# Kernel tuning notes

Hardware: AMD Instinct MI355X
Metric: run time of the kernel (lower is better)

The kernel has to match this reference:

```python
import jax, jax.numpy as jnp
import numpy as np

KERNEL_SIZE = 257

def conv1d_same_padding(x, weights):
    # x: [B,1,L], weights: [K]  (cross-correlation, matching torch F.conv1d)
    K = weights.shape[0]
    pad_total = K - 1
    if pad_total % 2 != 0:
        x = jnp.pad(x, ((0, 0), (0, 0), (0, 1)))
    p = pad_total // 2
    w = weights.reshape(1, 1, K)  # [out_ch, in_ch, K]
    return jax.lax.conv_general_dilated(
        x, w, window_strides=(1,), padding=[(p, p)],
        dimension_numbers=('NCW', 'OIW', 'NCW'))

def topk_absolutes_1d(x, k):
    # keep top-k |values| per sample, zero the rest (scatter semantics of repo)
    B = x.shape[0]
    xf = x.reshape(B, -1)
    _, idx = jax.lax.top_k(jnp.abs(xf), k)            # [B, k]
    vals = jnp.take_along_axis(xf, idx, axis=-1)      # [B, k]
    out = jnp.zeros_like(xf).at[jnp.arange(B)[:, None], idx].set(vals)
    return out.reshape(x.shape)

def setup_inputs() -> dict:
    key = jax.random.key(0)
    k1, k2 = jax.random.split(key)
    x = jax.random.normal(k1, (64, 1, 262144), dtype=jnp.float32)
    weights = jax.random.normal(k2, (KERNEL_SIZE,), dtype=jnp.float32) * 0.1
    return {"x": x, "weights": weights, "k": 2048}

def reference(x, weights, k):
    similarity = conv1d_same_padding(x, weights)
    extrema = topk_absolutes_1d(similarity, k)
    reconstruction = conv1d_same_padding(extrema, weights)
    return (reconstruction, similarity, extrema)
```

## Files before the change

kernel.cpp:

```cpp
#include <hip/hip_runtime.h>

#define L_LEN 262144
#define KSZ 257
#define BLK 256
#define R 16
#define TILE (BLK * R)
#define HALO (KSZ - 1)
#define LDSA (TILE + HALO)
#define NBIN 4096
#define SEGCAP 256
#define NCHUNK 32
#define CANDMAX 4096
#define TIECAP 1024

#define LDSW 4368
#define NJ 9

typedef __attribute__((ext_vector_type(8))) short bf16x8;
typedef __attribute__((ext_vector_type(4))) float f32x4;

__device__ __forceinline__ ushort bf16_rne(float f) {
    const unsigned u = __float_as_uint(f);
    return (ushort)((u + 0x7FFFu + ((u >> 16) & 1u)) >> 16);
}

__global__ __launch_bounds__(BLK) void zero_ghist_kernel(uint4* __restrict__ p) {
    p[(size_t)blockIdx.x * BLK + threadIdx.x] = make_uint4(0u, 0u, 0u, 0u);
}

__global__ __launch_bounds__(BLK) void conv_hist_kernel(const float* __restrict__ in,
                                                        const float* __restrict__ w,
                                                        float* __restrict__ out,
                                                        unsigned* __restrict__ ghist) {
    __shared__ float lx[LDSA + LDSA / 16];
    __shared__ unsigned shist[NBIN];
    const int t = threadIdx.x;
    const int sample = blockIdx.x >> 6;
    const int tile   = blockIdx.x & 63;
    const float* xrow = in  + (size_t)sample * L_LEN;
    float*       orow = out + (size_t)sample * L_LEN;
    const int tstart = tile * TILE;
    const int gbase  = tstart - (KSZ / 2);

    for (int h = t; h < NBIN; h += BLK) shist[h] = 0u;

    for (int i4 = t; i4 < LDSA / 4; i4 += BLK) {
        const int g = gbase + i4 * 4;
        float4 v;
        if ((unsigned)g <= (unsigned)(L_LEN - 4)) v = *(const float4*)(xrow + g);
        else v = make_float4(0.f, 0.f, 0.f, 0.f);
        const int ib = i4 * 4;
        const int p = ib + (ib >> 4);
        lx[p]     = v.x; lx[p + 1] = v.y; lx[p + 2] = v.z; lx[p + 3] = v.w;
    }
    __syncthreads();

    const int pb = t * 17;
    float acc[R], win[R];
#pragma unroll
    for (int r = 0; r < R; ++r) acc[r] = 0.f;
#pragma unroll
    for (int p = 0; p < R; ++p) win[p] = lx[pb + p];

#pragma unroll 1
    for (int j0 = 0; j0 < KSZ - 1; j0 += R) {
        const int pj = pb + j0 + (j0 >> 4) + 17;
#pragma unroll
        for (int jj = 0; jj < R; ++jj) {
            const float wj = w[j0 + jj];
#pragma unroll
            for (int r = 0; r < R; ++r)
                acc[r] += win[(jj + r) & (R - 1)] * wj;
            win[jj] = lx[pj + jj];
        }
    }
    const float wl = w[KSZ - 1];
#pragma unroll
    for (int r = 0; r < R; ++r) acc[r] += win[r] * wl;

#pragma unroll
    for (int r4 = 0; r4 < R; r4 += 4)
        *(float4*)(orow + tstart + t * R + r4) =
            make_float4(acc[r4], acc[r4 + 1], acc[r4 + 2], acc[r4 + 3]);

#pragma unroll
    for (int r = 0; r < R; ++r) {
        const unsigned u = (__float_as_uint(acc[r]) & 0x7fffffffu) >> 19;
        atomicAdd(&shist[u], 1u);
    }
    __syncthreads();
    for (int h = t; h < NBIN; h += BLK) {
        const unsigned c = shist[h];
        if (c) atomicAdd(&ghist[(size_t)sample * NBIN + h], c);
    }
}

__global__ __launch_bounds__(BLK) void mfma_recon_kernel(const float* __restrict__ in,
                                                         const float* __restrict__ w,
                                                         float* __restrict__ out) {
    __shared__ ushort xh[LDSW];
    __shared__ ushort xl[LDSW];

    const int t = threadIdx.x;
    const int sample = blockIdx.x >> 6;
    const int tile   = blockIdx.x & 63;
    const float* xrow = in  + (size_t)sample * L_LEN;
    float*       orow = out + (size_t)sample * L_LEN;
    const int tstart = tile * TILE;
    const int gbase  = tstart - (KSZ / 2);

    for (int i4 = t; i4 < LDSW / 4; i4 += BLK) {
        const int g = gbase + i4 * 4;
        float4 v;
        if ((unsigned)g <= (unsigned)(L_LEN - 4)) v = *(const float4*)(xrow + g);
        else v = make_float4(0.f, 0.f, 0.f, 0.f);
        const float vv[4] = {v.x, v.y, v.z, v.w};
        ushort h4[4], l4[4];
#pragma unroll
        for (int e = 0; e < 4; ++e) {
            const ushort h = bf16_rne(vv[e]);
            h4[e] = h;
            l4[e] = bf16_rne(vv[e] - __uint_as_float((unsigned)h << 16));
        }
        *(ushort4*)(&xh[i4 * 4]) = make_ushort4(h4[0], h4[1], h4[2], h4[3]);
        *(ushort4*)(&xl[i4 * 4]) = make_ushort4(l4[0], l4[1], l4[2], l4[3]);
    }

    const int lane = t & 63;
    const int cc = lane & 15;
    const int bb = lane >> 4;
    bf16x8 Bh[NJ], Bl[NJ];
#pragma unroll
    for (int f = 0; f < NJ; ++f) {
#pragma unroll
        for (int e = 0; e < 8; ++e) {
            const int j = f * 32 + 8 * bb + e - cc;
            const float v = ((unsigned)j <= 256u) ? w[j] : 0.f;
            const ushort h = bf16_rne(v);
            Bh[f][e] = (short)h;
            Bl[f][e] = (short)bf16_rne(v - __uint_as_float((unsigned)h << 16));
        }
    }
    __syncthreads();

    const int wv = t >> 6;
    const int wvbase = wv * 1024;
    const int arow = 16 * cc + 8 * bb;

    f32x4 acc[4] = {};
#pragma unroll
    for (int f = 0; f < NJ; ++f) {
#pragma unroll
        for (int st = 0; st < 4; ++st) {
            const int ao = wvbase + st * 256 + f * 32 + arow;
            const bf16x8 Ah = *(const bf16x8*)(&xh[ao]);
            const bf16x8 Al = *(const bf16x8*)(&xl[ao]);
            acc[st] = __builtin_amdgcn_mfma_f32_16x16x32_bf16(Ah, Bh[f], acc[st], 0, 0, 0);
            acc[st] = __builtin_amdgcn_mfma_f32_16x16x32_bf16(Ah, Bl[f], acc[st], 0, 0, 0);
            acc[st] = __builtin_amdgcn_mfma_f32_16x16x32_bf16(Al, Bh[f], acc[st], 0, 0, 0);
        }
    }

#pragma unroll
    for (int st = 0; st < 4; ++st) {
        const int mbase = tstart + wvbase + st * 256 + 64 * bb + cc;
#pragma unroll
        for (int r = 0; r < 4; ++r)
            orow[mbase + 16 * r] = acc[st][r];
    }
}

__global__ __launch_bounds__(1024) void bin_select_kernel(const unsigned* __restrict__ ghist,
                                                          int2* __restrict__ sel,
                                                          const int* __restrict__ kptr) {
    __shared__ int ss[1024];
    const int t = threadIdx.x;
    const int b = blockIdx.x;
    const unsigned* hist = ghist + (size_t)b * NBIN;
    const int k = kptr[0];

    const int g4 = t * 4;
    const int h0 = (int)hist[g4], h1 = (int)hist[g4 + 1],
              h2 = (int)hist[g4 + 2], h3 = (int)hist[g4 + 3];
    ss[t] = h0 + h1 + h2 + h3;
    __syncthreads();
    for (int off = 1; off < 1024; off <<= 1) {
        const int add = (t + off < 1024) ? ss[t + off] : 0;
        __syncthreads();
        ss[t] += add;
        __syncthreads();
    }
    const int S0 = ss[t];
    const int S4 = (t < 1023) ? ss[t + 1] : 0;
    const int S1 = S0 - h0, S2 = S1 - h1, S3 = S2 - h2;
    if (S0 >= k && S1 < k) sel[b] = make_int2(g4,     k - S1);
    if (S1 >= k && S2 < k) sel[b] = make_int2(g4 + 1, k - S2);
    if (S2 >= k && S3 < k) sel[b] = make_int2(g4 + 2, k - S3);
    if (S3 >= k && S4 < k) sel[b] = make_int2(g4 + 3, k - S4);
}

__global__ __launch_bounds__(BLK) void write_gather_kernel(const float* __restrict__ sim,
                                                           float* __restrict__ ext,
                                                           uint2* __restrict__ cand,
                                                           int* __restrict__ segCnt,
                                                           const int2* __restrict__ sel) {
    __shared__ int s_cnt;
    const int t = threadIdx.x;
    const int b = blockIdx.x >> 5;
    const int chunk = blockIdx.x & (NCHUNK - 1);
    const unsigned selBin = (unsigned)sel[b].x;
    const float* row  = sim + (size_t)b * L_LEN;
    float*       erow = ext + (size_t)b * L_LEN;
    uint2* seg = cand + ((size_t)b * NCHUNK + chunk) * SEGCAP;
    const int base = chunk * (L_LEN / NCHUNK);

    if (t == 0) s_cnt = 0;
    __syncthreads();

    for (int i = t; i < (L_LEN / NCHUNK) / 4; i += BLK) {
        const int g = base + i * 4;
        const float4 v = *(const float4*)(row + g);
        const float vv[4] = {v.x, v.y, v.z, v.w};
        float o[4];
#pragma unroll
        for (int e = 0; e < 4; ++e) {
            const unsigned u = __float_as_uint(vv[e]) & 0x7fffffffu;
            const unsigned u12 = u >> 19;
            o[e] = (u12 > selBin) ? vv[e] : 0.f;
            if (u12 == selBin) {
                const int p = atomicAdd(&s_cnt, 1);
                if (p < SEGCAP) seg[p] = make_uint2(u, (unsigned)(g + e));
            }
        }
        *(float4*)(erow + g) = make_float4(o[0], o[1], o[2], o[3]);
    }
    __syncthreads();
    if (t == 0) segCnt[b * NCHUNK + chunk] = (s_cnt < SEGCAP) ? s_cnt : SEGCAP;
}

__global__ __launch_bounds__(1024) void finalize_kernel(const float* __restrict__ sim,
                                                        float* __restrict__ ext,
                                                        const uint2* __restrict__ cand,
                                                        const int* __restrict__ segCnt,
                                                        const int2* __restrict__ sel) {
    __shared__ int hist[1024];
    __shared__ int ss[1024];
    __shared__ uint2 list[CANDMAX];
    __shared__ int tie[TIECAP];
    __shared__ int scnt[NCHUNK];
    __shared__ int segoff[NCHUNK + 1];
    __shared__ int s_b1, s_kk2, s_Tlow, s_m, s_tieCnt;
    const int t = threadIdx.x;
    const int b = blockIdx.x;
    const float* srow = sim + (size_t)b * L_LEN;
    float*       erow = ext + (size_t)b * L_LEN;
    const int kk = sel[b].y;

    if (t < NCHUNK) scnt[t] = segCnt[b * NCHUNK + t];
    __syncthreads();
    if (t == 0) {
        int acc0 = 0;
        for (int s = 0; s < NCHUNK; ++s) { segoff[s] = acc0; acc0 += scnt[s]; }
        segoff[NCHUNK] = acc0;
    }
    if (t == 1) s_tieCnt = 0;
    __syncthreads();
    int cnt = segoff[NCHUNK]; if (cnt > CANDMAX) cnt = CANDMAX;

    for (int j = t; j < NCHUNK * SEGCAP; j += 1024) {
        const int s = j >> 8;
        const int i = j & (SEGCAP - 1);
        if (i < scnt[s]) {
            const int dst = segoff[s] + i;
            if (dst < CANDMAX)
                list[dst] = cand[((size_t)b * NCHUNK + s) * SEGCAP + i];
        }
    }
    __syncthreads();

    hist[t] = 0;
    __syncthreads();
    for (int p = t; p < cnt; p += 1024)
        atomicAdd(&hist[(list[p].x & 0x7FFFFu) >> 9], 1);
    __syncthreads();
    ss[t] = hist[t];
    __syncthreads();
    for (int off = 1; off < 1024; off <<= 1) {
        const int add = (t + off < 1024) ? ss[t + off] : 0;
        __syncthreads();
        ss[t] += add;
        __syncthreads();
    }
    {
        const int S = ss[t];
        const int Sn = (t < 1023) ? ss[t + 1] : 0;
        if (S >= kk && Sn < kk) { s_b1 = t; s_kk2 = kk - Sn; }
    }
    __syncthreads();
    const int b1 = s_b1, kk2 = s_kk2;

    if (t < 512) hist[t] = 0;
    __syncthreads();
    for (int p = t; p < cnt; p += 1024) {
        const unsigned u19 = list[p].x & 0x7FFFFu;
        if ((int)(u19 >> 9) == b1) atomicAdd(&hist[u19 & 511u], 1);
    }
    __syncthreads();
    if (t < 512) ss[t] = hist[t];
    __syncthreads();
    for (int off = 1; off < 512; off <<= 1) {
        const int add = (t < 512 && t + off < 512) ? ss[t + off] : 0;
        __syncthreads();
        if (t < 512) ss[t] += add;
        __syncthreads();
    }
    if (t < 512) {
        const int S = ss[t];
        const int Sn = (t < 511) ? ss[t + 1] : 0;
        if (S >= kk2 && Sn < kk2) { s_Tlow = (b1 << 9) | t; s_m = kk2 - Sn; }
    }
    __syncthreads();
    const unsigned Tlow = (unsigned)s_Tlow;
    const int m = s_m;

    for (int p = t; p < cnt; p += 1024) {
        const unsigned u19 = list[p].x & 0x7FFFFu;
        const int idx = (int)list[p].y;
        if (u19 > Tlow) erow[idx] = srow[idx];
        else if (u19 == Tlow) {
            const int q = atomicAdd(&s_tieCnt, 1);
            if (q < TIECAP) tie[q] = idx;
        }
    }
    __syncthreads();
    int tc = s_tieCnt; if (tc > TIECAP) tc = TIECAP;
    for (int p = t; p < tc; p += 1024) {
        const int idx = tie[p];
        int rank = 0;
        for (int q = 0; q < tc; ++q) rank += (tie[q] < idx) ? 1 : 0;
        if (rank < m) erow[idx] = srow[idx];
    }
}

extern "C" void kernel_launch(void* const* d_in, const int* in_sizes, int n_in,
                              void* d_out, int out_size, void* d_ws, size_t ws_size,
                              hipStream_t stream) {
    const float* x    = (const float*)d_in[0];
    const float* w    = (const float*)d_in[1];
    const int*   kptr = (const int*)d_in[2];
    float* out = (float*)d_out;

    const int total = in_sizes[0];
    const int B = total / L_LEN;

    float* recon = out;
    float* sim   = out + (size_t)total;
    float* ext   = out + 2 * (size_t)total;

    uint8_t* ws = (uint8_t*)d_ws;
    unsigned* ghist  = (unsigned*)ws;
    int2*     sel    = (int2*)(ws + 1048576);
    int*      segCnt = (int*)(ws + 1048576 + 512);
    uint2*    cand   = (uint2*)(ws + 1048576 + 512 + 8192);

    zero_ghist_kernel<<<dim3((B * NBIN * 4) / (16 * BLK)), BLK, 0, stream>>>((uint4*)ghist);

    conv_hist_kernel<<<dim3(B * 64), BLK, 0, stream>>>(x, w, sim, ghist);
    bin_select_kernel<<<dim3(B), 1024, 0, stream>>>(ghist, sel, kptr);
    write_gather_kernel<<<dim3(B * NCHUNK), BLK, 0, stream>>>(sim, ext, cand, segCnt, sel);
    finalize_kernel<<<dim3(B), 1024, 0, stream>>>(sim, ext, cand, segCnt, sel);
    mfma_recon_kernel<<<dim3(B * 64), BLK, 0, stream>>>(ext, w, recon);
}
```

Before: 177.7 us.

## Compute similarity conv with split-bf16 MFMA and refine near-threshold values in fp32

```diff
diff --git a/kernel.cpp b/kernel.cpp
--- a/kernel.cpp
+++ b/kernel.cpp
@@ -3,14 +3,13 @@
 #define L_LEN 262144
 #define KSZ 257
 #define BLK 256
-#define R 16
-#define TILE (BLK * R)
+#define TILE 4096
 #define HALO (KSZ - 1)
 #define LDSA (TILE + HALO)
 #define NBIN 4096
 #define SEGCAP 256
 #define NCHUNK 32
-#define CANDMAX 4096
+#define CANDMAX 6144
 #define TIECAP 1024
 
 #define LDSW 4368
@@ -24,16 +23,20 @@
     return (ushort)((u + 0x7FFFu + ((u >> 16) & 1u)) >> 16);
 }
 
-__global__ __launch_bounds__(BLK) void zero_ghist_kernel(uint4* __restrict__ p) {
-    p[(size_t)blockIdx.x * BLK + threadIdx.x] = make_uint4(0u, 0u, 0u, 0u);
-}
-
-__global__ __launch_bounds__(BLK) void conv_hist_kernel(const float* __restrict__ in,
+__global__ __launch_bounds__(BLK) void zero_ws_kernel(uint4* __restrict__ p, int n16) {
+    const int i = blockIdx.x * BLK + threadIdx.x;
+    if (i < n16) p[i] = make_uint4(0u, 0u, 0u, 0u);
+}
+
+template<bool HIST>
+__global__ __launch_bounds__(BLK) void mfma_conv_kernel(const float* __restrict__ in,
                                                         const float* __restrict__ w,
                                                         float* __restrict__ out,
                                                         unsigned* __restrict__ ghist) {
-    __shared__ float lx[LDSA + LDSA / 16];
-    __shared__ unsigned shist[NBIN];
+    __shared__ ushort xh[LDSW];
+    __shared__ ushort xl[LDSW];
+    __shared__ unsigned shist[HIST ? NBIN : 1];
+
     const int t = threadIdx.x;
     const int sample = blockIdx.x >> 6;
     const int tile   = blockIdx.x & 63;
@@ -42,8 +45,129 @@
     const int tstart = tile * TILE;
     const int gbase  = tstart - (KSZ / 2);
 
-    for (int h = t; h < NBIN; h += BLK) shist[h] = 0u;
-
+    if (HIST) for (int h = t; h < NBIN; h += BLK) shist[h] = 0u;
+
+    for (int i4 = t; i4 < LDSW / 4; i4 += BLK) {
+        const int g = gbase + i4 * 4;
+        float4 v;
+        if ((unsigned)g <= (unsigned)(L_LEN - 4)) v = *(const float4*)(xrow + g);
+        else v = make_float4(0.f, 0.f, 0.f, 0.f);
+        const float vv[4] = {v.x, v.y, v.z, v.w};
+        ushort h4[4], l4[4];
+#pragma unroll
+        for (int e = 0; e < 4; ++e) {
+            const ushort h = bf16_rne(vv[e]);
+            h4[e] = h;
+            l4[e] = bf16_rne(vv[e] - __uint_as_float((unsigned)h << 16));
+        }
+        *(ushort4*)(&xh[i4 * 4]) = make_ushort4(h4[0], h4[1], h4[2], h4[3]);
+        *(ushort4*)(&xl[i4 * 4]) = make_ushort4(l4[0], l4[1], l4[2], l4[3]);
+    }
+
+    const int lane = t & 63;
+    const int cc = lane & 15;
+    const int bb = lane >> 4;
+    bf16x8 Bh[NJ], Bl[NJ];
+#pragma unroll
+    for (int f = 0; f < NJ; ++f) {
+#pragma unroll
+        for (int e = 0; e < 8; ++e) {
+            const int j = f * 32 + 8 * bb + e - cc;
+            const float v = ((unsigned)j <= 256u) ? w[j] : 0.f;
+            const ushort h = bf16_rne(v);
+            Bh[f][e] = (short)h;
+            Bl[f][e] = (short)bf16_rne(v - __uint_as_float((unsigned)h << 16));
+        }
+    }
+    __syncthreads();
+
+    const int wv = t >> 6;
+    const int wvbase = wv * 1024;
+    const int arow = 16 * cc + 8 * bb;
+
+    f32x4 acc[4] = {};
+#pragma unroll
+    for (int f = 0; f < NJ; ++f) {
+#pragma unroll
+        for (int st = 0; st < 4; ++st) {
+            const int ao = wvbase + st * 256 + f * 32 + arow;
+            const bf16x8 Ah = *(const bf16x8*)(&xh[ao]);
+            const bf16x8 Al = *(const bf16x8*)(&xl[ao]);
+            acc[st] = __builtin_amdgcn_mfma_f32_16x16x32_bf16(Ah, Bh[f], acc[st], 0, 0, 0);
+            acc[st] = __builtin_amdgcn_mfma_f32_16x16x32_bf16(Ah, Bl[f], acc[st], 0, 0, 0);
+            acc[st] = __builtin_amdgcn_mfma_f32_16x16x32_bf16(Al, Bh[f], acc[st], 0, 0, 0);
+        }
+    }
+
+#pragma unroll
+    for (int st = 0; st < 4; ++st) {
+        const int mbase = tstart + wvbase + st * 256 + 64 * bb + cc;
+#pragma unroll
+        for (int r = 0; r < 4; ++r) {
+            const float v = acc[st][r];
+            orow[mbase + 16 * r] = v;
+            if (HIST) {
+                const unsigned u = (__float_as_uint(v) & 0x7fffffffu) >> 19;
+                atomicAdd(&shist[u], 1u);
+            }
+        }
+    }
+
+    if (HIST) {
+        __syncthreads();
+        for (int h = t; h < NBIN; h += BLK) {
+            const unsigned c = shist[h];
+            if (c) atomicAdd(&ghist[(size_t)sample * NBIN + h], c);
+        }
+    }
+}
+
+__global__ __launch_bounds__(1024) void bin_select_kernel(const unsigned* __restrict__ ghist,
+                                                          int2* __restrict__ sel,
+                                                          const int* __restrict__ kptr) {
+    __shared__ int ss[1024];
+    const int t = threadIdx.x;
+    const int b = blockIdx.x;
+    const unsigned* hist = ghist + (size_t)b * NBIN;
+    const int k = kptr[0];
+
+    const int g4 = t * 4;
+    const int h0 = (int)hist[g4], h1 = (int)hist[g4 + 1],
+              h2 = (int)hist[g4 + 2], h3 = (int)hist[g4 + 3];
+    ss[t] = h0 + h1 + h2 + h3;
+    __syncthreads();
+    for (int off = 1; off < 1024; off <<= 1) {
+        const int add = (t + off < 1024) ? ss[t + off] : 0;
+        __syncthreads();
+        ss[t] += add;
+        __syncthreads();
+    }
+    const int S0 = ss[t];
+    const int S4 = (t < 1023) ? ss[t + 1] : 0;
+    const int S1 = S0 - h0, S2 = S1 - h1, S3 = S2 - h2;
+    if (S0 >= k && S1 < k) sel[b] = make_int2(g4,     k - S1);
+    if (S1 >= k && S2 < k) sel[b] = make_int2(g4 + 1, k - S2);
+    if (S2 >= k && S3 < k) sel[b] = make_int2(g4 + 2, k - S3);
+    if (S3 >= k && S4 < k) sel[b] = make_int2(g4 + 3, k - S4);
+}
+
+__global__ __launch_bounds__(BLK) void refine_kernel(const float* __restrict__ in,
+                                                     const float* __restrict__ w,
+                                                     float* __restrict__ sim,
+                                                     const int2* __restrict__ sel,
+                                                     int* __restrict__ delta) {
+    __shared__ float lx[LDSA + LDSA / 16];
+    __shared__ float lw[KSZ];
+    const int t = threadIdx.x;
+    const int sample = blockIdx.x >> 6;
+    const int tile   = blockIdx.x & 63;
+    const float* xrow = in  + (size_t)sample * L_LEN;
+    float*       srow = sim + (size_t)sample * L_LEN;
+    const int tstart = tile * TILE;
+    const int gbase  = tstart - (KSZ / 2);
+    const unsigned selBin = (unsigned)sel[sample].x;
+
+    for (int i = t; i < KSZ; i += BLK) lw[i] = w[i];
     for (int i4 = t; i4 < LDSA / 4; i4 += BLK) {
         const int g = gbase + i4 * 4;
         float4 v;
@@ -51,152 +175,33 @@
         else v = make_float4(0.f, 0.f, 0.f, 0.f);
         const int ib = i4 * 4;
         const int p = ib + (ib >> 4);
-        lx[p]     = v.x; lx[p + 1] = v.y; lx[p + 2] = v.z; lx[p + 3] = v.w;
-    }
-    __syncthreads();
-
-    const int pb = t * 17;
-    float acc[R], win[R];
-#pragma unroll
-    for (int r = 0; r < R; ++r) acc[r] = 0.f;
-#pragma unroll
-    for (int p = 0; p < R; ++p) win[p] = lx[pb + p];
-
-#pragma unroll 1
-    for (int j0 = 0; j0 < KSZ - 1; j0 += R) {
-        const int pj = pb + j0 + (j0 >> 4) + 17;
-#pragma unroll
-        for (int jj = 0; jj < R; ++jj) {
-            const float wj = w[j0 + jj];
-#pragma unroll
-            for (int r = 0; r < R; ++r)
-                acc[r] += win[(jj + r) & (R - 1)] * wj;
-            win[jj] = lx[pj + jj];
-        }
-    }
-    const float wl = w[KSZ - 1];
-#pragma unroll
-    for (int r = 0; r < R; ++r) acc[r] += win[r] * wl;
-
-#pragma unroll
-    for (int r4 = 0; r4 < R; r4 += 4)
-        *(float4*)(orow + tstart + t * R + r4) =
-            make_float4(acc[r4], acc[r4 + 1], acc[r4 + 2], acc[r4 + 3]);
-
-#pragma unroll
-    for (int r = 0; r < R; ++r) {
-        const unsigned u = (__float_as_uint(acc[r]) & 0x7fffffffu) >> 19;
-        atomicAdd(&shist[u], 1u);
-    }
-    __syncthreads();
-    for (int h = t; h < NBIN; h += BLK) {
-        const unsigned c = shist[h];
-        if (c) atomicAdd(&ghist[(size_t)sample * NBIN + h], c);
-    }
-}
-
-__global__ __launch_bounds__(BLK) void mfma_recon_kernel(const float* __restrict__ in,
-                                                         const float* __restrict__ w,
-                                                         float* __restrict__ out) {
-    __shared__ ushort xh[LDSW];
-    __shared__ ushort xl[LDSW];
-
-    const int t = threadIdx.x;
-    const int sample = blockIdx.x >> 6;
-    const int tile   = blockIdx.x & 63;
-    const float* xrow = in  + (size_t)sample * L_LEN;
-    float*       orow = out + (size_t)sample * L_LEN;
-    const int tstart = tile * TILE;
-    const int gbase  = tstart - (KSZ / 2);
-
-    for (int i4 = t; i4 < LDSW / 4; i4 += BLK) {
-        const int g = gbase + i4 * 4;
-        float4 v;
-        if ((unsigned)g <= (unsigned)(L_LEN - 4)) v = *(const float4*)(xrow + g);
-        else v = make_float4(0.f, 0.f, 0.f, 0.f);
-        const float vv[4] = {v.x, v.y, v.z, v.w};
-        ushort h4[4], l4[4];
+        lx[p] = v.x; lx[p + 1] = v.y; lx[p + 2] = v.z; lx[p + 3] = v.w;
+    }
+    __syncthreads();
+
+#pragma unroll
+    for (int q = 0; q < 4; ++q) {
+        const int m0 = t * 16 + q * 4;
+        const float4 sv = *(const float4*)(srow + tstart + m0);
+        const float vv[4] = {sv.x, sv.y, sv.z, sv.w};
 #pragma unroll
         for (int e = 0; e < 4; ++e) {
-            const ushort h = bf16_rne(vv[e]);
-            h4[e] = h;
-            l4[e] = bf16_rne(vv[e] - __uint_as_float((unsigned)h << 16));
-        }
-        *(ushort4*)(&xh[i4 * 4]) = make_ushort4(h4[0], h4[1], h4[2], h4[3]);
-        *(ushort4*)(&xl[i4 * 4]) = make_ushort4(l4[0], l4[1], l4[2], l4[3]);
-    }
-
-    const int lane = t & 63;
-    const int cc = lane & 15;
-    const int bb = lane >> 4;
-    bf16x8 Bh[NJ], Bl[NJ];
-#pragma unroll
-    for (int f = 0; f < NJ; ++f) {
-#pragma unroll
-        for (int e = 0; e < 8; ++e) {
-            const int j = f * 32 + 8 * bb + e - cc;
-            const float v = ((unsigned)j <= 256u) ? w[j] : 0.f;
-            const ushort h = bf16_rne(v);
-            Bh[f][e] = (short)h;
-            Bl[f][e] = (short)bf16_rne(v - __uint_as_float((unsigned)h << 16));
-        }
-    }
-    __syncthreads();
-
-    const int wv = t >> 6;
-    const int wvbase = wv * 1024;
-    const int arow = 16 * cc + 8 * bb;
-
-    f32x4 acc[4] = {};
-#pragma unroll
-    for (int f = 0; f < NJ; ++f) {
-#pragma unroll
-        for (int st = 0; st < 4; ++st) {
-            const int ao = wvbase + st * 256 + f * 32 + arow;
-            const bf16x8 Ah = *(const bf16x8*)(&xh[ao]);
-            const bf16x8 Al = *(const bf16x8*)(&xl[ao]);
-            acc[st] = __builtin_amdgcn_mfma_f32_16x16x32_bf16(Ah, Bh[f], acc[st], 0, 0, 0);
-            acc[st] = __builtin_amdgcn_mfma_f32_16x16x32_bf16(Ah, Bl[f], acc[st], 0, 0, 0);
-            acc[st] = __builtin_amdgcn_mfma_f32_16x16x32_bf16(Al, Bh[f], acc[st], 0, 0, 0);
-        }
-    }
-
-#pragma unroll
-    for (int st = 0; st < 4; ++st) {
-        const int mbase = tstart + wvbase + st * 256 + 64 * bb + cc;
-#pragma unroll
-        for (int r = 0; r < 4; ++r)
-            orow[mbase + 16 * r] = acc[st][r];
-    }
-}
-
-__global__ __launch_bounds__(1024) void bin_select_kernel(const unsigned* __restrict__ ghist,
-                                                          int2* __restrict__ sel,
-                                                          const int* __restrict__ kptr) {
-    __shared__ int ss[1024];
-    const int t = threadIdx.x;
-    const int b = blockIdx.x;
-    const unsigned* hist = ghist + (size_t)b * NBIN;
-    const int k = kptr[0];
-
-    const int g4 = t * 4;
-    const int h0 = (int)hist[g4], h1 = (int)hist[g4 + 1],
-              h2 = (int)hist[g4 + 2], h3 = (int)hist[g4 + 3];
-    ss[t] = h0 + h1 + h2 + h3;
-    __syncthreads();
-    for (int off = 1; off < 1024; off <<= 1) {
-        const int add = (t + off < 1024) ? ss[t + off] : 0;
-        __syncthreads();
-        ss[t] += add;
-        __syncthreads();
-    }
-    const int S0 = ss[t];
-    const int S4 = (t < 1023) ? ss[t + 1] : 0;
-    const int S1 = S0 - h0, S2 = S1 - h1, S3 = S2 - h2;
-    if (S0 >= k && S1 < k) sel[b] = make_int2(g4,     k - S1);
-    if (S1 >= k && S2 < k) sel[b] = make_int2(g4 + 1, k - S2);
-    if (S2 >= k && S3 < k) sel[b] = make_int2(g4 + 2, k - S3);
-    if (S3 >= k && S4 < k) sel[b] = make_int2(g4 + 3, k - S4);
+            const unsigned u12 = (__float_as_uint(vv[e]) & 0x7fffffffu) >> 19;
+            if ((unsigned)(u12 + 1u - selBin) <= 2u) {
+                const int ml = m0 + e;
+                float acc = 0.f;
+                for (int j = 0; j < KSZ; ++j) {
+                    const int el = ml + j;
+                    acc = fmaf(lw[j], lx[el + (el >> 4)], acc);
+                }
+                const unsigned pu = (__float_as_uint(acc) & 0x7fffffffu) >> 19;
+                const int pre_gt  = (u12 > selBin) ? 1 : 0;
+                const int post_gt = (pu  > selBin) ? 1 : 0;
+                if (pre_gt != post_gt) atomicAdd(&delta[sample], post_gt - pre_gt);
+                srow[tstart + ml] = acc;
+            }
+        }
+    }
 }
 
 __global__ __launch_bounds__(BLK) void write_gather_kernel(const float* __restrict__ sim,
@@ -227,7 +232,7 @@
             const unsigned u = __float_as_uint(vv[e]) & 0x7fffffffu;
             const unsigned u12 = u >> 19;
             o[e] = (u12 > selBin) ? vv[e] : 0.f;
-            if (u12 == selBin) {
+            if ((unsigned)(selBin - u12) <= 1u) {
                 const int p = atomicAdd(&s_cnt, 1);
                 if (p < SEGCAP) seg[p] = make_uint2(u, (unsigned)(g + e));
             }
@@ -242,7 +247,8 @@
                                                         float* __restrict__ ext,
                                                         const uint2* __restrict__ cand,
                                                         const int* __restrict__ segCnt,
-                                                        const int2* __restrict__ sel) {
+                                                        const int2* __restrict__ sel,
+                                                        const int* __restrict__ delta) {
     __shared__ int hist[1024];
     __shared__ int ss[1024];
     __shared__ uint2 list[CANDMAX];
@@ -254,18 +260,22 @@
     const int b = blockIdx.x;
     const float* srow = sim + (size_t)b * L_LEN;
     float*       erow = ext + (size_t)b * L_LEN;
-    const int kk = sel[b].y;
+    const unsigned selBin = (unsigned)sel[b].x;
+    const unsigned vbase = (selBin > 0 ? selBin - 1 : 0) << 19;
+    int kk = sel[b].y - delta[b];
 
     if (t < NCHUNK) scnt[t] = segCnt[b * NCHUNK + t];
     __syncthreads();
     if (t == 0) {
-        int acc0 = 0;
-        for (int s = 0; s < NCHUNK; ++s) { segoff[s] = acc0; acc0 += scnt[s]; }
-        segoff[NCHUNK] = acc0;
+        int a = 0;
+        for (int s = 0; s < NCHUNK; ++s) { segoff[s] = a; a += scnt[s]; }
+        segoff[NCHUNK] = a;
     }
     if (t == 1) s_tieCnt = 0;
     __syncthreads();
     int cnt = segoff[NCHUNK]; if (cnt > CANDMAX) cnt = CANDMAX;
+    if (kk <= 0) return;
+    if (kk > cnt) kk = cnt;
 
     for (int j = t; j < NCHUNK * SEGCAP; j += 1024) {
         const int s = j >> 8;
@@ -281,7 +291,7 @@
     hist[t] = 0;
     __syncthreads();
     for (int p = t; p < cnt; p += 1024)
-        atomicAdd(&hist[(list[p].x & 0x7FFFFu) >> 9], 1);
+        atomicAdd(&hist[(list[p].x - vbase) >> 10], 1);
     __syncthreads();
     ss[t] = hist[t];
     __syncthreads();
@@ -299,35 +309,35 @@
     __syncthreads();
     const int b1 = s_b1, kk2 = s_kk2;
 
-    if (t < 512) hist[t] = 0;
+    hist[t] = 0;
     __syncthreads();
     for (int p = t; p < cnt; p += 1024) {
-        const unsigned u19 = list[p].x & 0x7FFFFu;
-        if ((int)(u19 >> 9) == b1) atomicAdd(&hist[u19 & 511u], 1);
-    }
-    __syncthreads();
-    if (t < 512) ss[t] = hist[t];
-    __syncthreads();
-    for (int off = 1; off < 512; off <<= 1) {
-        const int add = (t < 512 && t + off < 512) ? ss[t + off] : 0;
-        __syncthreads();
-        if (t < 512) ss[t] += add;
-        __syncthreads();
-    }
-    if (t < 512) {
+        const unsigned v = list[p].x - vbase;
+        if ((int)(v >> 10) == b1) atomicAdd(&hist[v & 1023u], 1);
+    }
+    __syncthreads();
+    ss[t] = hist[t];
+    __syncthreads();
+    for (int off = 1; off < 1024; off <<= 1) {
+        const int add = (t + off < 1024) ? ss[t + off] : 0;
+        __syncthreads();
+        ss[t] += add;
+        __syncthreads();
+    }
+    {
         const int S = ss[t];
-        const int Sn = (t < 511) ? ss[t + 1] : 0;
-        if (S >= kk2 && Sn < kk2) { s_Tlow = (b1 << 9) | t; s_m = kk2 - Sn; }
+        const int Sn = (t < 1023) ? ss[t + 1] : 0;
+        if (S >= kk2 && Sn < kk2) { s_Tlow = (b1 << 10) | t; s_m = kk2 - Sn; }
     }
     __syncthreads();
     const unsigned Tlow = (unsigned)s_Tlow;
     const int m = s_m;
 
     for (int p = t; p < cnt; p += 1024) {
-        const unsigned u19 = list[p].x & 0x7FFFFu;
+        const unsigned v = list[p].x - vbase;
         const int idx = (int)list[p].y;
-        if (u19 > Tlow) erow[idx] = srow[idx];
-        else if (u19 == Tlow) {
+        if (v > Tlow) erow[idx] = srow[idx];
+        else if (v == Tlow) {
             const int q = atomicAdd(&s_tieCnt, 1);
             if (q < TIECAP) tie[q] = idx;
         }
@@ -359,15 +369,18 @@
 
     uint8_t* ws = (uint8_t*)d_ws;
     unsigned* ghist  = (unsigned*)ws;
-    int2*     sel    = (int2*)(ws + 1048576);
-    int*      segCnt = (int*)(ws + 1048576 + 512);
-    uint2*    cand   = (uint2*)(ws + 1048576 + 512 + 8192);
-
-    zero_ghist_kernel<<<dim3((B * NBIN * 4) / (16 * BLK)), BLK, 0, stream>>>((uint4*)ghist);
-
-    conv_hist_kernel<<<dim3(B * 64), BLK, 0, stream>>>(x, w, sim, ghist);
+    int*      delta  = (int*)(ws + 1048576);
+    int2*     sel    = (int2*)(ws + 1048576 + 1024);
+    int*      segCnt = (int*)(ws + 1048576 + 2048);
+    uint2*    cand   = (uint2*)(ws + 1048576 + 2048 + 8192);
+
+    const int n16 = (1048576 + 1024) / 16;
+    zero_ws_kernel<<<dim3((n16 + BLK - 1) / BLK), BLK, 0, stream>>>((uint4*)ws, n16);
+
+    mfma_conv_kernel<true><<<dim3(B * 64), BLK, 0, stream>>>(x, w, sim, ghist);
     bin_select_kernel<<<dim3(B), 1024, 0, stream>>>(ghist, sel, kptr);
+    refine_kernel<<<dim3(B * 64), BLK, 0, stream>>>(x, w, sim, sel, delta);
     write_gather_kernel<<<dim3(B * NCHUNK), BLK, 0, stream>>>(sim, ext, cand, segCnt, sel);
-    finalize_kernel<<<dim3(B), 1024, 0, stream>>>(sim, ext, cand, segCnt, sel);
-    mfma_recon_kernel<<<dim3(B * 64), BLK, 0, stream>>>(ext, w, recon);
-}
+    finalize_kernel<<<dim3(B), 1024, 0, stream>>>(sim, ext, cand, segCnt, sel, delta);
+    mfma_conv_kernel<false><<<dim3(B * 64), BLK, 0, stream>>>(ext, w, recon, nullptr);
+}
```

Result: slower. 445.9 us (+150.9%).
